# Kernel tuning notes

Hardware: AMD Instinct MI355X
Metric: run time of the kernel (lower is better)

The kernel has to match this reference:

```python
import jax, jax.numpy as jnp
import numpy as np
from functools import partial

N_NODES = 50000
N_EDGES = 1_600_000
T = 9
F_IN = 128
HID = 128
OUT = 1


def setup_inputs() -> dict:
    key = jax.random.key(0)
    ks = jax.random.split(key, 8)
    s = 0.05
    return {
        "x_seq": jax.random.normal(ks[0], (T, N_NODES, F_IN), dtype=jnp.float32),
        "edge_index": jax.random.randint(ks[1], (2, N_EDGES), 0, N_NODES, dtype=jnp.int64),
        "W_gcn": jax.random.normal(ks[2], (F_IN, HID), dtype=jnp.float32) * s,
        "b_gcn": jnp.zeros((HID,), dtype=jnp.float32),
        "W_ih": jax.random.normal(ks[3], (4 * HID, HID), dtype=jnp.float32) * s,
        "W_hh": jax.random.normal(ks[4], (4 * HID, HID), dtype=jnp.float32) * s,
        "b_ih": jnp.zeros((4 * HID,), dtype=jnp.float32),
        "b_hh": jnp.zeros((4 * HID,), dtype=jnp.float32),
        "W_fc": jax.random.normal(ks[5], (HID, OUT), dtype=jnp.float32) * s,
        "b_fc": jnp.zeros((OUT,), dtype=jnp.float32),
    }


def reference(x_seq, edge_index, W_gcn, b_gcn, W_ih, W_hh, b_ih, b_hh, W_fc, b_fc):
    T_, N, _ = x_seq.shape
    H = W_hh.shape[1]

    # --- GCNConv normalization (add self-loops, symmetric deg^-1/2) ---
    loops = jnp.arange(N, dtype=edge_index.dtype)
    src = jnp.concatenate([edge_index[0], loops])  # [E+N]
    dst = jnp.concatenate([edge_index[1], loops])  # [E+N]
    deg = jax.ops.segment_sum(jnp.ones_like(dst, dtype=x_seq.dtype), dst, num_segments=N)
    dinv = jnp.where(deg > 0, jax.lax.rsqrt(deg), 0.0)
    norm = dinv[src] * dinv[dst]  # [E+N]

    # Linear transform for all timesteps at once (dense GEMM)
    xw = jnp.einsum("tnf,fh->tnh", x_seq, W_gcn)  # [T, N, H]

    # Per-timestep gather -> scale -> scatter-add (scan to bound memory)
    def gcn_step(_, xw_t):
        msg = xw_t[src] * norm[:, None]                       # [E+N, H]
        agg = jax.ops.segment_sum(msg, dst, num_segments=N)   # [N, H]
        return None, jax.nn.relu(agg + b_gcn)                 # dropout: eval mode (identity)

    _, emb = jax.lax.scan(gcn_step, None, xw)  # [T, N, H]

    # --- single-layer LSTM over time, nodes as batch (PyTorch gate order i,f,g,o) ---
    def lstm_step(carry, x_t):
        h_prev, c_prev = carry
        gates = x_t @ W_ih.T + h_prev @ W_hh.T + (b_ih + b_hh)  # [N, 4H]
        i, f, g, o = jnp.split(gates, 4, axis=-1)
        i, f, o = jax.nn.sigmoid(i), jax.nn.sigmoid(f), jax.nn.sigmoid(o)
        g = jnp.tanh(g)
        c = f * c_prev + i * g
        h = o * jnp.tanh(c)
        return (h, c), h

    init = (jnp.zeros((N, H), x_seq.dtype), jnp.zeros((N, H), x_seq.dtype))
    _, hs = jax.lax.scan(lstm_step, init, emb)  # [T, N, H]

    lstm_out = jnp.transpose(hs, (1, 0, 2))  # [N, T, H] (batch_first)
    # final_dropout: eval mode (identity)
    return lstm_out @ W_fc + b_fc  # [N, T, OUT]
```

## Files before the change

kernel.cpp:

```cpp
#include <hip/hip_runtime.h>
#include <math.h>

#define NN 50000
#define TT 9
#define FD 128
#define HD 128

using short8 = __attribute__((ext_vector_type(8))) short;
using half8  = __attribute__((ext_vector_type(8))) _Float16;
using f32x4  = __attribute__((ext_vector_type(4))) float;
using f32x2  = __attribute__((ext_vector_type(2))) float;
using half2v = __attribute__((ext_vector_type(2))) _Float16;
typedef unsigned short ushort_t;

__device__ inline unsigned short f2bf(float x) {
  unsigned int u = __float_as_uint(x);
  unsigned int r = (u + 0x7fffu + ((u >> 16) & 1u)) >> 16;
  return (unsigned short)r;
}
__device__ inline float bf2f(unsigned short h) {
  return __uint_as_float(((unsigned int)h) << 16);
}
__device__ inline void split2(float x, unsigned short& h, unsigned short& l) {
  h = f2bf(x);
  l = f2bf(x - bf2f(h));
}
__device__ inline float fast_sigmoid(float x) {
  x = fminf(fmaxf(x, -30.f), 30.f);
  return 1.f / (1.f + __expf(-x));
}
__device__ inline float fast_tanh(float x) {
  x = fminf(fmaxf(x, -15.f), 15.f);
  float e = __expf(2.f * x);
  return (e - 1.f) / (e + 1.f);
}

__global__ void k_detect(const unsigned int* __restrict__ e32, int nchk,
                         int* __restrict__ stride_out) {
  __shared__ unsigned int red[256];
  unsigned int acc = 0;
  for (int i = threadIdx.x; i < nchk; i += 256) acc |= e32[2 * i + 1];
  red[threadIdx.x] = acc;
  __syncthreads();
  for (int s = 128; s > 0; s >>= 1) {
    if ((int)threadIdx.x < s) red[threadIdx.x] |= red[threadIdx.x + s];
    __syncthreads();
  }
  if (threadIdx.x == 0) stride_out[0] = (red[0] == 0u) ? 2 : 1;
}

__global__ void k_count(const unsigned int* __restrict__ e32, int E,
                        const int* __restrict__ stridep, int* __restrict__ cnt) {
  int e = blockIdx.x * 256 + threadIdx.x;
  if (e >= E) return;
  int st = stridep[0];
  int d = (int)e32[(size_t)(E + e) * st];
  atomicAdd(&cnt[d], 1);
}

__global__ void k_dinv(const int* __restrict__ cnt, float* __restrict__ dinv, int N) {
  int n = blockIdx.x * 256 + threadIdx.x;
  if (n < N) dinv[n] = rsqrtf((float)(cnt[n] + 1));
}

__global__ void k_scan(const int* __restrict__ cnt, int* __restrict__ rowp, int N) {
  __shared__ int buf[1024];
  __shared__ int carry_s;
  if (threadIdx.x == 0) carry_s = 0;
  __syncthreads();
  for (int base = 0; base < N; base += 1024) {
    int i = base + threadIdx.x;
    int v = (i < N) ? cnt[i] : 0;
    buf[threadIdx.x] = v;
    __syncthreads();
    for (int off = 1; off < 1024; off <<= 1) {
      int t = ((int)threadIdx.x >= off) ? buf[threadIdx.x - off] : 0;
      __syncthreads();
      buf[threadIdx.x] += t;
      __syncthreads();
    }
    int incl = buf[threadIdx.x];
    int carry = carry_s;
    if (i < N) rowp[i] = carry + incl - v;
    __syncthreads();
    if (threadIdx.x == 1023) carry_s = carry + incl;
    __syncthreads();
  }
  if (threadIdx.x == 0) rowp[N] = carry_s;
}

__global__ void k_scatter(const unsigned int* __restrict__ e32, int E,
                          const int* __restrict__ stridep, const int* __restrict__ rowp,
                          int* __restrict__ fill, int* __restrict__ col) {
  int e = blockIdx.x * 256 + threadIdx.x;
  if (e >= E) return;
  int st = stridep[0];
  int s = (int)e32[(size_t)e * st];
  int d = (int)e32[(size_t)(E + e) * st];
  int pos = rowp[d] + atomicAdd(&fill[d], 1);
  col[pos] = s;
}

__global__ __launch_bounds__(256) void k_prep(const float* __restrict__ x,
                                              const float* __restrict__ dinv,
                                              _Float16* __restrict__ xs) {
  int lane = threadIdx.x & 63;
  int n = blockIdx.x * 4 + (threadIdx.x >> 6);
  int t = blockIdx.y;
  float dn = dinv[n];
  f32x2 v = __builtin_nontemporal_load(
      (const f32x2*)(x + ((size_t)t * NN + n) * 128 + lane * 2));
  half2v r;
  r.x = (_Float16)(v.x * dn);
  r.y = (_Float16)(v.y * dn);
  *(half2v*)(xs + ((size_t)t * NN + n) * 128 + lane * 2) = r;
}

__global__ void k_packw(const float* __restrict__ Wih, const float* __restrict__ Whh,
                        const float* __restrict__ bih, const float* __restrict__ bhh,
                        ushort_t* __restrict__ Wh_, ushort_t* __restrict__ Wl_,
                        float* __restrict__ bsum) {
  int r = blockIdx.x;
  int k = threadIdx.x;
  int ri = (r & 127) * 4 + (r >> 7);
  float v = (k < 128) ? Wih[(size_t)r * 128 + k] : Whh[(size_t)r * 128 + (k - 128)];
  unsigned short h, l;
  split2(v, h, l);
  size_t o = ((size_t)(k >> 3) * 512 + ri) * 8 + (k & 7);
  Wh_[o] = h;
  Wl_[o] = l;
  if (k == 0) bsum[ri] = bih[r] + bhh[r];
}

__global__ void k_packg(const float* __restrict__ Wg, _Float16* __restrict__ Gh_,
                        _Float16* __restrict__ Gl_) {
  int h = blockIdx.x, k = threadIdx.x;
  float v = Wg[(size_t)k * 128 + h];
  _Float16 hi = (_Float16)v;
  _Float16 lo = (_Float16)(v - (float)hi);
  size_t o = ((size_t)(k >> 3) * 128 + h) * 8 + (k & 7);
  Gh_[o] = hi;
  Gl_[o] = lo;
}

__global__ __launch_bounds__(256) void k_agg(const _Float16* __restrict__ xs,
                                             const float* __restrict__ dinv,
                                             const int* __restrict__ rowp,
                                             const int* __restrict__ col,
                                             _Float16* __restrict__ agg16) {
  __shared__ unsigned int pk[4][132];
  int lane = threadIdx.x & 63;
  int wv = threadIdx.x >> 6;
  int n = blockIdx.x * 4 + wv;
  int t = blockIdx.y;
  const _Float16* xb = xs + (size_t)t * NN * 128;
  float dn = dinv[n];
  half2v sv = *(const half2v*)(xb + (size_t)n * 128 + lane * 2);
  float ax = (float)sv.x, ay = (float)sv.y;
  int beg = rowp[n], end = rowp[n + 1];
  for (int base = beg; base < end; base += 64) {
    int m = end - base;
    if (m > 64) m = 64;
    int sl = (lane < m) ? col[base + lane] : 0;
    int j = 0;
    for (; j + 8 <= m; j += 8) {
      int s[8];
#pragma unroll
      for (int u = 0; u < 8; ++u) s[u] = __shfl(sl, j + u);
      half2v g[8];
#pragma unroll
      for (int u = 0; u < 8; ++u)
        g[u] = *(const half2v*)(xb + (size_t)s[u] * 128 + lane * 2);
#pragma unroll
      for (int u = 0; u < 8; ++u) {
        ax += (float)g[u].x;
        ay += (float)g[u].y;
      }
    }
    for (; j < m; ++j) {
      int s = __shfl(sl, j);
      half2v g = *(const half2v*)(xb + (size_t)s * 128 + lane * 2);
      ax += (float)g.x;
      ay += (float)g.y;
    }
  }
  half2v r;
  r.x = (_Float16)(ax * dn);
  r.y = (_Float16)(ay * dn);
  union { half2v h; unsigned int u; } cv;
  cv.h = r;
  pk[wv][lane] = cv.u;
  __syncthreads();
  int tid = threadIdx.x;
  if (tid < 64) {
    int g = tid & 3, c = tid >> 2;
    uint4 u4;
    u4.x = pk[g][c * 4 + 0];
    u4.y = pk[g][c * 4 + 1];
    u4.z = pk[g][c * 4 + 2];
    u4.w = pk[g][c * 4 + 3];
    int n2 = blockIdx.x * 4 + g;
    *(uint4*)(agg16 + ((size_t)(c * 9 + t) * NN + n2) * 8) = u4;
  }
}

#define BN 96
#define LST 136
__global__ __launch_bounds__(512, 2) void k_fused(
    const _Float16* __restrict__ agg16, const _Float16* __restrict__ Gh_,
    const _Float16* __restrict__ Gl_, const float* __restrict__ bg,
    const ushort_t* __restrict__ Wh_, const ushort_t* __restrict__ Wl_,
    const float* __restrict__ bsum, const float* __restrict__ Wfc,
    const float* __restrict__ bfc, float* __restrict__ out) {
  __shared__ ushort_t ldsEh[BN * LST];
  __shared__ ushort_t ldsEl[BN * LST];
  __shared__ ushort_t ldsHh[BN * LST];
  __shared__ ushort_t ldsHl[BN * LST];
  __shared__ float obuf[8][BN];
  int tid = threadIdx.x;
  int w = tid >> 6, lane = tid & 63, q = lane >> 4, cl = lane & 15;
  int n0 = blockIdx.x * BN;
  float cst[4][6] = {};
  float bfv = bfc[0];
#pragma unroll 1
  for (int t = 0; t < TT; ++t) {
    {
      f32x4 acce[6] = {};
#pragma unroll 2
      for (int ks = 0; ks < 4; ++ks) {
        int chunk = ks * 4 + q;
        size_t wo = ((size_t)chunk * 128 + w * 16 + cl) * 8;
        half8 gah = *(const half8*)(Gh_ + wo);
        half8 gal = *(const half8*)(Gl_ + wo);
#pragma unroll
        for (int ct = 0; ct < 6; ++ct) {
          int node = n0 + ct * 16 + cl;
          half8 b = {0, 0, 0, 0, 0, 0, 0, 0};
          if (node < NN)
            b = *(const half8*)(agg16 + ((size_t)(chunk * 9 + t) * NN + node) * 8);
          acce[ct] = __builtin_amdgcn_mfma_f32_16x16x32_f16(gah, b, acce[ct], 0, 0, 0);
          acce[ct] = __builtin_amdgcn_mfma_f32_16x16x32_f16(gal, b, acce[ct], 0, 0, 0);
        }
      }
#pragma unroll
      for (int ct = 0; ct < 6; ++ct) {
#pragma unroll
        for (int j = 0; j < 4; ++j) {
          int hid = w * 16 + q * 4 + j;
          float v = acce[ct][j] + bg[hid];
          v = v > 0.f ? v : 0.f;
          unsigned short hh, hl;
          split2(v, hh, hl);
          int ro = (ct * 16 + cl) * LST + hid;
          ldsEh[ro] = hh;
          ldsEl[ro] = hl;
        }
      }
    }
    __syncthreads();
    f32x4 acc[4][6] = {};
    int ksmax = (t == 0) ? 4 : 8;
#pragma unroll 2
    for (int ks = 0; ks < ksmax; ++ks) {
      int chunk = ks * 4 + q;
      const ushort_t* Bh = (ks < 4) ? ldsEh : ldsHh;
      const ushort_t* Bl = (ks < 4) ? ldsEl : ldsHl;
      int kk = (ks & 3) * 32 + q * 8;
      short8 bh[6], bl[6];
#pragma unroll
      for (int ct = 0; ct < 6; ++ct) {
        int ro = (ct * 16 + cl) * LST + kk;
        bh[ct] = *(const short8*)(Bh + ro);
        bl[ct] = *(const short8*)(Bl + ro);
      }
#pragma unroll
      for (int rt = 0; rt < 4; ++rt) {
        size_t ao = ((size_t)chunk * 512 + w * 64 + rt * 16 + cl) * 8;
        short8 ah = *(const short8*)(Wh_ + ao);
        short8 al = *(const short8*)(Wl_ + ao);
#pragma unroll
        for (int ct = 0; ct < 6; ++ct) {
          acc[rt][ct] = __builtin_amdgcn_mfma_f32_16x16x32_bf16(ah, bh[ct], acc[rt][ct], 0, 0, 0);
          acc[rt][ct] = __builtin_amdgcn_mfma_f32_16x16x32_bf16(ah, bl[ct], acc[rt][ct], 0, 0, 0);
          acc[rt][ct] = __builtin_amdgcn_mfma_f32_16x16x32_bf16(al, bh[ct], acc[rt][ct], 0, 0, 0);
        }
      }
    }
    __syncthreads();
    float op[6] = {0.f, 0.f, 0.f, 0.f, 0.f, 0.f};
#pragma unroll
    for (int rt = 0; rt < 4; ++rt) {
      int jl = w * 16 + rt * 4 + q;
      float4 bs = *(const float4*)(bsum + jl * 4);
      float wf = Wfc[jl];
#pragma unroll
      for (int ct = 0; ct < 6; ++ct) {
        float gi = acc[rt][ct][0] + bs.x;
        float gf = acc[rt][ct][1] + bs.y;
        float gg = acc[rt][ct][2] + bs.z;
        float go = acc[rt][ct][3] + bs.w;
        float ig = fast_sigmoid(gi), fg = fast_sigmoid(gf), og = fast_sigmoid(go);
        float gt = fast_tanh(gg);
        float cn = fg * cst[rt][ct] + ig * gt;
        cst[rt][ct] = cn;
        float hn = og * fast_tanh(cn);
        op[ct] += hn * wf;
        unsigned short hh, hl;
        split2(hn, hh, hl);
        int ro = (ct * 16 + cl) * LST + jl;
        ldsHh[ro] = hh;
        ldsHl[ro] = hl;
      }
    }
#pragma unroll
    for (int ct = 0; ct < 6; ++ct) {
      op[ct] += __shfl_xor(op[ct], 16);
      op[ct] += __shfl_xor(op[ct], 32);
    }
    if (q == 0) {
#pragma unroll
      for (int ct = 0; ct < 6; ++ct) obuf[w][ct * 16 + cl] = op[ct];
    }
    __syncthreads();
    if (tid < BN) {
      int node = n0 + tid;
      if (node < NN) {
        float v = bfv;
#pragma unroll
        for (int ww = 0; ww < 8; ++ww) v += obuf[ww][tid];
        out[(size_t)node * TT + t] = v;
      }
    }
  }
}

static inline size_t alignup(size_t x) { return (x + 511) & ~(size_t)511; }

extern "C" void kernel_launch(void* const* d_in, const int* in_sizes, int n_in,
                              void* d_out, int out_size, void* d_ws, size_t ws_size,
                              hipStream_t stream) {
  const float* x_seq = (const float*)d_in[0];
  const unsigned int* e32 = (const unsigned int*)d_in[1];
  const float* W_gcn = (const float*)d_in[2];
  const float* b_gcn = (const float*)d_in[3];
  const float* W_ih = (const float*)d_in[4];
  const float* W_hh = (const float*)d_in[5];
  const float* b_ih = (const float*)d_in[6];
  const float* b_hh = (const float*)d_in[7];
  const float* W_fc = (const float*)d_in[8];
  const float* b_fc = (const float*)d_in[9];
  float* out = (float*)d_out;

  const int N = NN;
  const int E = in_sizes[1] / 2;

  char* p = (char*)d_ws;
  int* stridep = (int*)p;                    p += 512;
  int* cnt = (int*)p;                        p += alignup((size_t)N * 4);
  int* rowp = (int*)p;                       p += alignup((size_t)(N + 1) * 4);
  int* col = (int*)p;                        p += alignup((size_t)E * 4);
  float* dinv = (float*)p;                   p += alignup((size_t)N * 4);
  _Float16* xs16 = (_Float16*)p;             p += alignup((size_t)9 * N * 128 * 2);
  _Float16* agg16 = (_Float16*)p;            p += alignup((size_t)16 * 9 * N * 8 * 2);
  ushort_t* wpkh = (ushort_t*)p;             p += alignup((size_t)32 * 512 * 8 * 2);
  ushort_t* wpkl = (ushort_t*)p;             p += alignup((size_t)32 * 512 * 8 * 2);
  _Float16* wgth = (_Float16*)p;             p += alignup((size_t)16 * 128 * 8 * 2);
  _Float16* wgtl = (_Float16*)p;             p += alignup((size_t)16 * 128 * 8 * 2);
  float* bsum = (float*)p;                   p += alignup((size_t)512 * 4);

  hipMemsetAsync(cnt, 0, (size_t)N * 4, stream);

  int nchk = E < 8192 ? E : 8192;
  k_detect<<<1, 256, 0, stream>>>(e32, nchk, stridep);
  k_count<<<(E + 255) / 256, 256, 0, stream>>>(e32, E, stridep, cnt);
  k_dinv<<<(N + 255) / 256, 256, 0, stream>>>(cnt, dinv, N);
  k_scan<<<1, 1024, 0, stream>>>(cnt, rowp, N);
  hipMemsetAsync(cnt, 0, (size_t)N * 4, stream);
  k_scatter<<<(E + 255) / 256, 256, 0, stream>>>(e32, E, stridep, rowp, cnt, col);
  k_prep<<<dim3(N / 4, 9), 256, 0, stream>>>(x_seq, dinv, xs16);
  k_packw<<<512, 256, 0, stream>>>(W_ih, W_hh, b_ih, b_hh, wpkh, wpkl, bsum);
  k_packg<<<128, 128, 0, stream>>>(W_gcn, wgth, wgtl);

  k_agg<<<dim3(N / 4, 9), 256, 0, stream>>>(xs16, dinv, rowp, col, agg16);
  k_fused<<<(N + BN - 1) / BN, 512, 0, stream>>>(agg16, wgth, wgtl, b_gcn,
                                                 wpkh, wpkl, bsum, W_fc, b_fc, out);
}
```

Before: 1.704 ms.

## Switch LSTM GEMM to fp16 two-term split and halve node tile

The LSTM gate GEMM moves from a three-product bf16 hi/lo split to fp16 MFMA, with the weights split into hi/lo halves and the activations (GCN embedding and hidden state) stored as single fp16 values. This removes one of the three MFMAs per tile and halves the LDS footprint for the activation buffers. The node tile per block drops from 96 to 48 and the launch bound rises to 4 blocks per CU, trading per-block reuse of weight loads for higher occupancy. Rounding activations to fp16 loses some precision relative to the previous split scheme.

```diff
diff --git a/kernel.cpp b/kernel.cpp
--- a/kernel.cpp
+++ b/kernel.cpp
@@ -13,18 +13,6 @@
 using half2v = __attribute__((ext_vector_type(2))) _Float16;
 typedef unsigned short ushort_t;
 
-__device__ inline unsigned short f2bf(float x) {
-  unsigned int u = __float_as_uint(x);
-  unsigned int r = (u + 0x7fffu + ((u >> 16) & 1u)) >> 16;
-  return (unsigned short)r;
-}
-__device__ inline float bf2f(unsigned short h) {
-  return __uint_as_float(((unsigned int)h) << 16);
-}
-__device__ inline void split2(float x, unsigned short& h, unsigned short& l) {
-  h = f2bf(x);
-  l = f2bf(x - bf2f(h));
-}
 __device__ inline float fast_sigmoid(float x) {
   x = fminf(fmaxf(x, -30.f), 30.f);
   return 1.f / (1.f + __expf(-x));
@@ -118,17 +106,17 @@
 
 __global__ void k_packw(const float* __restrict__ Wih, const float* __restrict__ Whh,
                         const float* __restrict__ bih, const float* __restrict__ bhh,
-                        ushort_t* __restrict__ Wh_, ushort_t* __restrict__ Wl_,
+                        _Float16* __restrict__ Wh_, _Float16* __restrict__ Wl_,
                         float* __restrict__ bsum) {
   int r = blockIdx.x;
   int k = threadIdx.x;
   int ri = (r & 127) * 4 + (r >> 7);
   float v = (k < 128) ? Wih[(size_t)r * 128 + k] : Whh[(size_t)r * 128 + (k - 128)];
-  unsigned short h, l;
-  split2(v, h, l);
+  _Float16 hi = (_Float16)v;
+  _Float16 lo = (_Float16)(v - (float)hi);
   size_t o = ((size_t)(k >> 3) * 512 + ri) * 8 + (k & 7);
-  Wh_[o] = h;
-  Wl_[o] = l;
+  Wh_[o] = hi;
+  Wl_[o] = lo;
   if (k == 0) bsum[ri] = bih[r] + bhh[r];
 }
 
@@ -204,28 +192,26 @@
   }
 }
 
-#define BN 96
+#define BN 48
 #define LST 136
-__global__ __launch_bounds__(512, 2) void k_fused(
+__global__ __launch_bounds__(512, 4) void k_fused(
     const _Float16* __restrict__ agg16, const _Float16* __restrict__ Gh_,
     const _Float16* __restrict__ Gl_, const float* __restrict__ bg,
-    const ushort_t* __restrict__ Wh_, const ushort_t* __restrict__ Wl_,
+    const _Float16* __restrict__ Wh_, const _Float16* __restrict__ Wl_,
     const float* __restrict__ bsum, const float* __restrict__ Wfc,
     const float* __restrict__ bfc, float* __restrict__ out) {
-  __shared__ ushort_t ldsEh[BN * LST];
-  __shared__ ushort_t ldsEl[BN * LST];
-  __shared__ ushort_t ldsHh[BN * LST];
-  __shared__ ushort_t ldsHl[BN * LST];
+  __shared__ _Float16 ldsE[BN * LST];
+  __shared__ _Float16 ldsH[BN * LST];
   __shared__ float obuf[8][BN];
   int tid = threadIdx.x;
   int w = tid >> 6, lane = tid & 63, q = lane >> 4, cl = lane & 15;
   int n0 = blockIdx.x * BN;
-  float cst[4][6] = {};
+  float cst[4][3] = {};
   float bfv = bfc[0];
 #pragma unroll 1
   for (int t = 0; t < TT; ++t) {
     {
-      f32x4 acce[6] = {};
+      f32x4 acce[3] = {};
 #pragma unroll 2
       for (int ks = 0; ks < 4; ++ks) {
         int chunk = ks * 4 + q;
@@ -233,7 +219,7 @@
         half8 gah = *(const half8*)(Gh_ + wo);
         half8 gal = *(const half8*)(Gl_ + wo);
 #pragma unroll
-        for (int ct = 0; ct < 6; ++ct) {
+        for (int ct = 0; ct < 3; ++ct) {
           int node = n0 + ct * 16 + cl;
           half8 b = {0, 0, 0, 0, 0, 0, 0, 0};
           if (node < NN)
@@ -243,58 +229,49 @@
         }
       }
 #pragma unroll
-      for (int ct = 0; ct < 6; ++ct) {
+      for (int ct = 0; ct < 3; ++ct) {
 #pragma unroll
         for (int j = 0; j < 4; ++j) {
           int hid = w * 16 + q * 4 + j;
           float v = acce[ct][j] + bg[hid];
           v = v > 0.f ? v : 0.f;
-          unsigned short hh, hl;
-          split2(v, hh, hl);
-          int ro = (ct * 16 + cl) * LST + hid;
-          ldsEh[ro] = hh;
-          ldsEl[ro] = hl;
+          ldsE[(ct * 16 + cl) * LST + hid] = (_Float16)v;
         }
       }
     }
     __syncthreads();
-    f32x4 acc[4][6] = {};
+    f32x4 acc[4][3] = {};
     int ksmax = (t == 0) ? 4 : 8;
 #pragma unroll 2
     for (int ks = 0; ks < ksmax; ++ks) {
       int chunk = ks * 4 + q;
-      const ushort_t* Bh = (ks < 4) ? ldsEh : ldsHh;
-      const ushort_t* Bl = (ks < 4) ? ldsEl : ldsHl;
+      const _Float16* Bp = (ks < 4) ? ldsE : ldsH;
       int kk = (ks & 3) * 32 + q * 8;
-      short8 bh[6], bl[6];
-#pragma unroll
-      for (int ct = 0; ct < 6; ++ct) {
-        int ro = (ct * 16 + cl) * LST + kk;
-        bh[ct] = *(const short8*)(Bh + ro);
-        bl[ct] = *(const short8*)(Bl + ro);
-      }
+      half8 bb[3];
+#pragma unroll
+      for (int ct = 0; ct < 3; ++ct)
+        bb[ct] = *(const half8*)(Bp + (ct * 16 + cl) * LST + kk);
 #pragma unroll
       for (int rt = 0; rt < 4; ++rt) {
         size_t ao = ((size_t)chunk * 512 + w * 64 + rt * 16 + cl) * 8;
-        short8 ah = *(const short8*)(Wh_ + ao);
-        short8 al = *(const short8*)(Wl_ + ao);
-#pragma unroll
-        for (int ct = 0; ct < 6; ++ct) {
-          acc[rt][ct] = __builtin_amdgcn_mfma_f32_16x16x32_bf16(ah, bh[ct], acc[rt][ct], 0, 0, 0);
-          acc[rt][ct] = __builtin_amdgcn_mfma_f32_16x16x32_bf16(ah, bl[ct], acc[rt][ct], 0, 0, 0);
-          acc[rt][ct] = __builtin_amdgcn_mfma_f32_16x16x32_bf16(al, bh[ct], acc[rt][ct], 0, 0, 0);
+        half8 ah = *(const half8*)(Wh_ + ao);
+        half8 al = *(const half8*)(Wl_ + ao);
+#pragma unroll
+        for (int ct = 0; ct < 3; ++ct) {
+          acc[rt][ct] = __builtin_amdgcn_mfma_f32_16x16x32_f16(ah, bb[ct], acc[rt][ct], 0, 0, 0);
+          acc[rt][ct] = __builtin_amdgcn_mfma_f32_16x16x32_f16(al, bb[ct], acc[rt][ct], 0, 0, 0);
         }
       }
     }
     __syncthreads();
-    float op[6] = {0.f, 0.f, 0.f, 0.f, 0.f, 0.f};
+    float op[3] = {0.f, 0.f, 0.f};
 #pragma unroll
     for (int rt = 0; rt < 4; ++rt) {
       int jl = w * 16 + rt * 4 + q;
       float4 bs = *(const float4*)(bsum + jl * 4);
       float wf = Wfc[jl];
 #pragma unroll
-      for (int ct = 0; ct < 6; ++ct) {
+      for (int ct = 0; ct < 3; ++ct) {
         float gi = acc[rt][ct][0] + bs.x;
         float gf = acc[rt][ct][1] + bs.y;
         float gg = acc[rt][ct][2] + bs.z;
@@ -305,21 +282,17 @@
         cst[rt][ct] = cn;
         float hn = og * fast_tanh(cn);
         op[ct] += hn * wf;
-        unsigned short hh, hl;
-        split2(hn, hh, hl);
-        int ro = (ct * 16 + cl) * LST + jl;
-        ldsHh[ro] = hh;
-        ldsHl[ro] = hl;
-      }
-    }
-#pragma unroll
-    for (int ct = 0; ct < 6; ++ct) {
+        ldsH[(ct * 16 + cl) * LST + jl] = (_Float16)hn;
+      }
+    }
+#pragma unroll
+    for (int ct = 0; ct < 3; ++ct) {
       op[ct] += __shfl_xor(op[ct], 16);
       op[ct] += __shfl_xor(op[ct], 32);
     }
     if (q == 0) {
 #pragma unroll
-      for (int ct = 0; ct < 6; ++ct) obuf[w][ct * 16 + cl] = op[ct];
+      for (int ct = 0; ct < 3; ++ct) obuf[w][ct * 16 + cl] = op[ct];
     }
     __syncthreads();
     if (tid < BN) {
@@ -362,8 +335,8 @@
   float* dinv = (float*)p;                   p += alignup((size_t)N * 4);
   _Float16* xs16 = (_Float16*)p;             p += alignup((size_t)9 * N * 128 * 2);
   _Float16* agg16 = (_Float16*)p;            p += alignup((size_t)16 * 9 * N * 8 * 2);
-  ushort_t* wpkh = (ushort_t*)p;             p += alignup((size_t)32 * 512 * 8 * 2);
-  ushort_t* wpkl = (ushort_t*)p;             p += alignup((size_t)32 * 512 * 8 * 2);
+  _Float16* wpkh = (_Float16*)p;             p += alignup((size_t)32 * 512 * 8 * 2);
+  _Float16* wpkl = (_Float16*)p;             p += alignup((size_t)32 * 512 * 8 * 2);
   _Float16* wgth = (_Float16*)p;             p += alignup((size_t)16 * 128 * 8 * 2);
   _Float16* wgtl = (_Float16*)p;             p += alignup((size_t)16 * 128 * 8 * 2);
   float* bsum = (float*)p;                   p += alignup((size_t)512 * 4);
```

Result: faster. 1.664 ms (-2.3%).
